# Kernel tuning notes

Measured on AMD Instinct MI355X. Metric: run time of the kernel, lower is better.

Reference implementation:

```python
import jax, jax.numpy as jnp
import numpy as np
from jax import lax

H, W = 128, 128
K_JUNC = 300
STEPS = 32
THRESH = 0.008
BIAS_SPAN = 1
SCALE = 5.0
SENTINEL = K_JUNC * K_JUNC


def decode_hafm(angs, dist, bias):
    # angs [B,3,H,W], dist [B,1,H,W], bias [B,1,H,W] -> lines [B,3,H,W,4]
    bias_range = jnp.arange(-BIAS_SPAN, BIAS_SPAN + 1, dtype=jnp.float32).reshape(1, -1, 1, 1)
    d = jnp.clip(dist + bias * bias_range, 0.0, 1.0)  # [B,3,H,W]
    angle0 = (angs[:, 0:1] - 0.5) * jnp.pi * 2
    angle1 = angs[:, 1:2] * jnp.pi / 2
    angle2 = -angs[:, 2:3] * jnp.pi / 2
    c0, s0 = jnp.cos(angle0), jnp.sin(angle0)
    t1, t2 = jnp.tan(angle1), jnp.tan(angle2)
    x1 = (c0 - s0 * t1) * d * SCALE
    y1 = (s0 + c0 * t1) * d * SCALE
    x2 = (c0 - s0 * t2) * d * SCALE
    y2 = (s0 + c0 * t2) * d * SCALE
    y0, x0 = jnp.meshgrid(jnp.arange(H, dtype=jnp.float32), jnp.arange(W, dtype=jnp.float32), indexing='ij')
    x0 = x0[None, None]
    y0 = y0[None, None]
    x1 = jnp.clip(x1 + x0, 0, W - 1)
    y1 = jnp.clip(y1 + y0, 0, H - 1)
    x2 = jnp.clip(x2 + x0, 0, W - 1)
    y2 = jnp.clip(y2 + y0, 0, H - 1)
    return jnp.stack((x1, y1, x2, y2), axis=-1)


def propose_junctions(jloc, joff):
    # jloc [H,W], joff [2,H,W]; 3x3 NMS + top-K, thresholded junctions
    pooled = lax.reduce_window(jloc, -jnp.inf, lax.max, (3, 3), (1, 1), 'SAME')
    nms = jnp.where(jloc == pooled, jloc, 0.0)
    scores, idx = lax.top_k(nms.reshape(-1), K_JUNC)
    y = (idx // W).astype(jnp.float32)
    x = (idx % W).astype(jnp.float32)
    xs = x + joff[0].reshape(-1)[idx]
    ys = y + joff[1].reshape(-1)[idx]
    coords = jnp.stack([xs, ys], axis=-1)  # [K,2]
    valid = scores > THRESH
    coords = jnp.where(valid[:, None], coords, 1e6)
    return coords, scores


def bilinear_sample(fmap, px, py):
    # fmap [C,H,W]; px,py [N,S] -> [C,N,S]
    C = fmap.shape[0]
    px = jnp.clip(px, 0.0, W - 1)
    py = jnp.clip(py, 0.0, H - 1)
    x0 = jnp.floor(px)
    y0 = jnp.floor(py)
    x0i = x0.astype(jnp.int32)
    y0i = y0.astype(jnp.int32)
    x1i = jnp.minimum(x0i + 1, W - 1)
    y1i = jnp.minimum(y0i + 1, H - 1)
    wx = px - x0
    wy = py - y0
    flat = fmap.reshape(C, H * W)

    def g(yi, xi):
        return flat[:, (yi * W + xi).reshape(-1)].reshape(C, *px.shape)

    return (g(y0i, x0i) * (1 - wx) * (1 - wy)
            + g(y0i, x1i) * wx * (1 - wy)
            + g(y1i, x0i) * (1 - wx) * wy
            + g(y1i, x1i) * wx * wy)


def setup_inputs() -> dict:
    key = jax.random.key(0)
    ks = jax.random.split(key, 10)
    return {
        'features': jax.random.normal(ks[0], (1, 256, H, W), jnp.float32),
        'heatmaps': jax.random.normal(ks[1], (1, 9, H, W), jnp.float32),
        'fc1_w': jax.random.normal(ks[2], (128, 256), jnp.float32) * 0.05,
        'fc1_b': jax.random.normal(ks[3], (128,), jnp.float32) * 0.05,
        'w1': jax.random.normal(ks[4], (1024, 1024), jnp.float32) * 0.03,
        'b1': jnp.zeros((1024,), jnp.float32),
        'w2': jax.random.normal(ks[5], (1024, 1024), jnp.float32) * 0.03,
        'b2': jnp.zeros((1024,), jnp.float32),
        'w3': jax.random.normal(ks[6], (1, 1024), jnp.float32) * 0.03,
        'b3': jnp.zeros((1,), jnp.float32),
    }


def reference(features, heatmaps, fc1_w, fc1_b, w1, b1, w2, b2, w3, b3):
    angs = jax.nn.sigmoid(heatmaps[:, 0:3])
    dist = jax.nn.sigmoid(heatmaps[:, 3:4])
    bias = jax.nn.sigmoid(heatmaps[:, 4:5])
    jloc = jax.nn.softmax(heatmaps[:, 5:7], axis=1)[0, 1]  # [H,W]
    joff = jax.nn.sigmoid(heatmaps[0, 7:9])                # [2,H,W]

    junc, _ = propose_junctions(jloc, joff)                # [K,2]
    lines = decode_hafm(angs, dist, bias).reshape(-1, 4)   # [N,4], N=3*H*W
    N = lines.shape[0]

    # junction-to-endpoint matching (cdist + argmin)
    d1 = ((junc[:, None, :] - lines[None, :, :2]) ** 2).sum(-1)  # [K,N]
    d2 = ((junc[:, None, :] - lines[None, :, 2:]) ** 2).sum(-1)
    j1 = jnp.argmin(d1, axis=0)
    j2 = jnp.argmin(d2, axis=0)
    lo = jnp.minimum(j1, j2)
    hi = jnp.maximum(j1, j2)
    ids = jnp.where(lo < hi, lo * K_JUNC + hi, SENTINEL)
    # fixed-size dedup (masked analogue of torch unique(dim=0))
    uids = jnp.unique(ids, size=N, fill_value=SENTINEL)
    valid = uids < SENTINEL
    uids_safe = jnp.where(valid, uids, 0)
    p1 = junc[uids_safe // K_JUNC]
    p2 = junc[uids_safe % K_JUNC]
    line_coords = jnp.where(valid[:, None], jnp.concatenate([p1, p2], axis=-1), 0.0)  # [N,4]

    # LOI feature sampling
    loi = jnp.einsum('oc,chw->ohw', fc1_w, features[0]) + fc1_b[:, None, None]  # [128,H,W]
    t = jnp.linspace(0.0, 1.0, STEPS)[None, :]
    px = line_coords[:, 0:1] * t + line_coords[:, 2:3] * (1 - t)  # [N,32]
    py = line_coords[:, 1:2] * t + line_coords[:, 3:4] * (1 - t)
    feats = bilinear_sample(loi, px, py)            # [128,N,32]
    feats = feats.transpose(1, 0, 2)                # [N,128,32]
    feats = feats.reshape(N, 128, STEPS // 4, 4).max(-1)  # max_pool1d k=4
    feats = feats.reshape(N, 1024)

    h = jax.nn.relu(feats @ w1.T + b1)
    h = jax.nn.relu(h @ w2.T + b2)
    logits = (h @ w3.T + b3)[:, 0]
    line_scores = jax.nn.sigmoid(logits) * valid
    return line_coords, line_scores
```

## Files before the change

kernel.cpp:

```cpp
#include <hip/hip_runtime.h>
#include <math.h>

#define HH 128
#define WW 128
#define HW 16384
#define NLINES 49152
#define KJ 300
#define SENT 90000
#define THRESHV 0.008f
#define CAND_CAP 4096
#define BITWORDS 2816

typedef __attribute__((ext_vector_type(8))) short bf16x8;
typedef __attribute__((ext_vector_type(4))) float f32x4;

__device__ __forceinline__ float sigm(float x){ return 1.0f/(1.0f+expf(-x)); }

__device__ __forceinline__ short tobf(float f){
  unsigned u = __float_as_uint(f);
  unsigned r = u + 0x7FFFu + ((u >> 16) & 1u);
  return (short)(r >> 16);
}
__device__ __forceinline__ float bflo(unsigned u){ return __uint_as_float(u << 16); }
__device__ __forceinline__ float bfhi(unsigned u){ return __uint_as_float(u & 0xFFFF0000u); }

#define GLOAD_LDS16(g, l) \
  __builtin_amdgcn_global_load_lds((const __attribute__((address_space(1))) void*)(g), \
                                   (__attribute__((address_space(3))) void*)(l), 16, 0, 0)

__device__ __forceinline__ float jloc_at(const float* hm, int idx){
  float h5 = hm[5*HW + idx], h6 = hm[6*HW + idx];
  float mx = fmaxf(h5,h6);
  float e5 = expf(h5-mx), e6 = expf(h6-mx);
  return e6/(e5+e6);
}

__global__ __launch_bounds__(256) void k_front(const float* __restrict__ hm,
    const float* __restrict__ feat, const float* __restrict__ fc1w,
    float* __restrict__ lines, unsigned long long* __restrict__ cand,
    int* __restrict__ cand_count, short* __restrict__ featT, short* __restrict__ fc1b16){
  __shared__ float tile[32][33];
  int b = blockIdx.x, t = threadIdx.x;
  if (b < 64){
    int i = b*256 + t;
    float h0 = hm[i], h1 = hm[HW+i], h2 = hm[2*HW+i], h3 = hm[3*HW+i], h4 = hm[4*HW+i];
    float a0 = sigm(h0), a1 = sigm(h1), a2 = sigm(h2);
    float dist = sigm(h3), bias = sigm(h4);
    const float PI = 3.14159265358979323846f;
    float ang0 = (a0-0.5f)*(2.0f*PI);
    float c0 = cosf(ang0), s0 = sinf(ang0);
    float t1 = tanf(a1*(0.5f*PI));
    float t2 = tanf(-a2*(0.5f*PI));
    int y = i >> 7, x = i & 127;
    float fx = (float)x, fy = (float)y;
    #pragma unroll
    for (int c=0;c<3;c++){
      float d = fminf(fmaxf(dist + bias*(float)(c-1), 0.0f), 1.0f);
      float ds = d*5.0f;
      float x1 = fminf(fmaxf((c0 - s0*t1)*ds + fx, 0.0f), 127.0f);
      float y1 = fminf(fmaxf((s0 + c0*t1)*ds + fy, 0.0f), 127.0f);
      float x2 = fminf(fmaxf((c0 - s0*t2)*ds + fx, 0.0f), 127.0f);
      float y2 = fminf(fmaxf((s0 + c0*t2)*ds + fy, 0.0f), 127.0f);
      ((float4*)lines)[c*HW + i] = make_float4(x1,y1,x2,y2);
    }
    float v = jloc_at(hm, i);
    float m = v;
    for (int dy=-1; dy<=1; dy++){
      int ny = y + dy; if (ny < 0 || ny >= HH) continue;
      for (int dx=-1; dx<=1; dx++){
        int nx = x + dx; if (nx < 0 || nx >= WW) continue;
        m = fmaxf(m, jloc_at(hm, ny*WW + nx));
      }
    }
    if (v == m && v > THRESHV){
      int pos = atomicAdd(cand_count, 1);
      if (pos < CAND_CAP){
        unsigned int vb = __float_as_uint(v);
        cand[pos] = ((unsigned long long)vb << 32) | (unsigned long long)(0xFFFFFFFFu - (unsigned)i);
      }
    }
  } else if (b < 64 + 4096){
    int idx = b - 64;
    int p0 = (idx & 511) * 32, c0 = (idx >> 9) * 32;
    int c  = t >> 3;
    int p4 = (t & 7) * 4;
    float4 v = *(const float4*)&feat[(size_t)(c0 + c)*HW + p0 + p4];
    tile[c][p4+0] = v.x; tile[c][p4+1] = v.y; tile[c][p4+2] = v.z; tile[c][p4+3] = v.w;
    __syncthreads();
    int p  = t >> 3;
    int cg = (t & 7) * 4;
    ushort4 o;
    o.x = (unsigned short)tobf(tile[cg+0][p]);
    o.y = (unsigned short)tobf(tile[cg+1][p]);
    o.z = (unsigned short)tobf(tile[cg+2][p]);
    o.w = (unsigned short)tobf(tile[cg+3][p]);
    *(ushort4*)&featT[(size_t)(p0 + p)*256 + c0 + cg] = o;
  } else {
    int j = (b - 4160)*256 + t;
    fc1b16[j] = tobf(fc1w[j]);
  }
}

__global__ __launch_bounds__(1024) void k_mid(
    const unsigned long long* __restrict__ cand, const int* __restrict__ cand_count,
    const float* __restrict__ hm, float* __restrict__ junc,
    const short* __restrict__ featT, const short* __restrict__ fc1b16,
    const float* __restrict__ fc1b, short* __restrict__ loi){
  __shared__ __align__(16) char smem[CAND_CAP*8];
  int b = blockIdx.x, t = threadIdx.x;
  if (b == 0){
    unsigned long long* s = (unsigned long long*)smem;
    int count = *cand_count; if (count > CAND_CAP) count = CAND_CAP;
    int n2 = 512;
    while (n2 < count) n2 <<= 1;
    for (int i=t; i<n2; i+=1024) s[i] = (i < count) ? cand[i] : 0ull;
    __syncthreads();
    for (int k=2; k<=n2; k<<=1){
      for (int j=k>>1; j>0; j>>=1){
        for (int i=t; i<n2; i+=1024){
          int ixj = i ^ j;
          if (ixj > i){
            unsigned long long a = s[i], bb = s[ixj];
            bool desc = ((i & k) == 0);
            if (desc ? (a < bb) : (a > bb)){ s[i] = bb; s[ixj] = a; }
          }
        }
        __syncthreads();
      }
    }
    if (t < KJ){
      float jx = 1e6f, jy = 1e6f;
      if (t < count){
        unsigned idx = 0xFFFFFFFFu - (unsigned)(s[t] & 0xFFFFFFFFull);
        int yy = (int)(idx >> 7), xx = (int)(idx & 127u);
        jx = (float)xx + sigm(hm[7*HW + idx]);
        jy = (float)yy + sigm(hm[8*HW + idx]);
      }
      junc[2*t] = jx; junc[2*t+1] = jy;
    }
  } else {
    if (t >= 256) return;
    short* As = (short*)smem;
    short* Bs = (short*)(smem + 8192);
    int rb = (b - 1) * 64;
    int lane = t & 63, wave = t >> 6;
    int l16 = lane & 15, quad = lane >> 4;
    int srow = lane >> 3, schunk = (lane & 7) ^ srow;
    f32x4 acc[8];
    #pragma unroll
    for (int g=0; g<8; g++) acc[g] = (f32x4){0,0,0,0};
    for (int k0=0; k0<256; k0+=64){
      #pragma unroll
      for (int i=0; i<2; i++){
        int r0 = wave*16 + i*8;
        GLOAD_LDS16(featT + (size_t)(rb + r0 + srow)*256 + k0 + schunk*8, &As[r0*64]);
      }
      #pragma unroll
      for (int i=0; i<4; i++){
        int r0 = wave*32 + i*8;
        GLOAD_LDS16(fc1b16 + (size_t)(r0 + srow)*256 + k0 + schunk*8, &Bs[r0*64]);
      }
      __syncthreads();
      #pragma unroll
      for (int s2=0; s2<2; s2++){
        int slot = (s2*4 + quad) ^ (l16 & 7);
        bf16x8 a = *(const bf16x8*)&As[(wave*16 + l16)*64 + slot*8];
        #pragma unroll
        for (int g=0; g<8; g++){
          bf16x8 bv = *(const bf16x8*)&Bs[(g*16 + l16)*64 + slot*8];
          acc[g] = __builtin_amdgcn_mfma_f32_16x16x32_bf16(a, bv, acc[g], 0, 0, 0);
        }
      }
      __syncthreads();
    }
    int rowbase = rb + wave*16 + quad*4;
    #pragma unroll
    for (int g=0; g<8; g++){
      int col = g*16 + l16;
      float bs = fc1b[col];
      #pragma unroll
      for (int r=0; r<4; r++)
        loi[(size_t)(rowbase + r)*128 + col] = tobf(acc[g][r] + bs);
    }
  }
}

__global__ __launch_bounds__(256) void k_match(const float* __restrict__ lines,
    const float* __restrict__ junc, int* __restrict__ ids,
    const float* __restrict__ w1, const float* __restrict__ w2,
    short* __restrict__ w1b, short* __restrict__ w2b){
  __shared__ float jx[KJ], jy[KJ];
  int b = blockIdx.x, t = threadIdx.x;
  if (b < 192){
    for (int k=t; k<KJ; k+=256){ jx[k] = junc[2*k]; jy[k] = junc[2*k+1]; }
    __syncthreads();
    int n = b*256 + t;
    float4 L = ((const float4*)lines)[n];
    float b1 = 1e30f, b2 = 1e30f; int j1 = 0, j2 = 0;
    #pragma unroll 4
    for (int k=0; k<KJ; k++){
      float dx1 = jx[k]-L.x, dy1 = jy[k]-L.y;
      float d1 = dx1*dx1 + dy1*dy1;
      float dx2 = jx[k]-L.z, dy2 = jy[k]-L.w;
      float d2 = dx2*dx2 + dy2*dy2;
      if (d1 < b1){ b1 = d1; j1 = k; }
      if (d2 < b2){ b2 = d2; j2 = k; }
    }
    int lo = min(j1,j2), hi = max(j1,j2);
    ids[n] = (lo < hi) ? (lo*KJ + hi) : SENT;
  } else {
    int j = (b - 192)*256 + t;
    w1b[j] = tobf(w1[j]);
    w2b[j] = tobf(w2[j]);
  }
}

__global__ __launch_bounds__(1024) void k_unique(const int* __restrict__ ids,
    int* __restrict__ uid_list, int* __restrict__ mcount){
  __shared__ unsigned bm[BITWORDS];
  __shared__ int wsum[16];
  int t = threadIdx.x;
  for (int i=t; i<BITWORDS; i+=1024) bm[i] = 0u;
  __syncthreads();
  for (int n=t; n<NLINES; n+=1024){
    int id = ids[n];
    if (id < SENT) atomicOr(&bm[id>>5], 1u << (id & 31));
  }
  __syncthreads();
  int w0 = t*3;
  int local = 0;
  unsigned wv[3];
  #pragma unroll
  for (int i=0; i<3; i++){
    int w = w0 + i;
    wv[i] = (w < BITWORDS) ? bm[w] : 0u;
    local += __popc(wv[i]);
  }
  int v = local;
  #pragma unroll
  for (int d=1; d<64; d<<=1){
    int nv = __shfl_up(v, d, 64);
    if ((t & 63) >= d) v += nv;
  }
  if ((t & 63) == 63) wsum[t >> 6] = v;
  __syncthreads();
  if (t < 16){
    int x = wsum[t];
    #pragma unroll
    for (int d=1; d<16; d<<=1){
      int nv = __shfl_up(x, d, 16);
      if (t >= d) x += nv;
    }
    wsum[t] = x;
  }
  __syncthreads();
  int base = v - local + ((t >> 6) ? wsum[(t >> 6) - 1] : 0);
  #pragma unroll
  for (int i=0; i<3; i++){
    unsigned bits = wv[i];
    while (bits){
      int bb = __ffs(bits) - 1;
      uid_list[base++] = (w0 + i)*32 + bb;
      bits &= bits - 1;
    }
  }
  if (t == 1023) *mcount = wsum[15];
}

__global__ __launch_bounds__(256) void k_sample(float* __restrict__ out,
    const int* __restrict__ uid_list, const float* __restrict__ junc,
    const short* __restrict__ loi, const int* __restrict__ mcount,
    short* __restrict__ fbuf, float* __restrict__ logit, int* __restrict__ cnt,
    int ncnt, int chunk0, int chunk){
  __shared__ int4   sOffs[32];
  __shared__ float4 sWts[32];
  int M = *mcount;
  int t = threadIdx.x;
  if (t == 0 && blockIdx.x < ncnt) cnt[blockIdx.x] = 0;
  int q  = t >> 6;
  int c2 = (t & 63) << 1;
  for (int l = blockIdx.x; l < chunk; l += gridDim.x){
    int r = chunk0 + l;
    if (r < M){
      if (t == 0) logit[l] = 0.0f;
      __syncthreads();
      if (t < 32){
        int id = uid_list[r];
        int lo = id / KJ, hi = id % KJ;
        float2 P1 = ((const float2*)junc)[lo];
        float2 P2 = ((const float2*)junc)[hi];
        if (t == 0) ((float4*)out)[r] = make_float4(P1.x, P1.y, P2.x, P2.y);
        float tt = (float)t * (1.0f/31.0f);
        float px = P1.x*tt + P2.x*(1.0f-tt);
        float py = P1.y*tt + P2.y*(1.0f-tt);
        px = fminf(fmaxf(px, 0.0f), 127.0f);
        py = fminf(fmaxf(py, 0.0f), 127.0f);
        float x0 = floorf(px), y0 = floorf(py);
        int x0i = (int)x0, y0i = (int)y0;
        int x1i = min(x0i+1, 127), y1i = min(y0i+1, 127);
        float wx = px - x0, wy = py - y0;
        sOffs[t] = make_int4((y0i*WW + x0i)*128, (y0i*WW + x1i)*128,
                             (y1i*WW + x0i)*128, (y1i*WW + x1i)*128);
        sWts[t]  = make_float4((1.0f-wx)*(1.0f-wy), wx*(1.0f-wy),
                               (1.0f-wx)*wy,        wx*wy);
      }
      __syncthreads();
      float gl0=-1e30f, gl1=-1e30f, gh0=-1e30f, gh1=-1e30f;
      #pragma unroll
      for (int j=0; j<8; j++){
        int s = q*8 + j;
        int4 o   = sOffs[s];
        float4 w = sWts[s];
        unsigned u00 = *(const unsigned*)&loi[o.x + c2];
        unsigned u01 = *(const unsigned*)&loi[o.y + c2];
        unsigned u10 = *(const unsigned*)&loi[o.z + c2];
        unsigned u11 = *(const unsigned*)&loi[o.w + c2];
        float vlo = w.x*bflo(u00) + w.y*bflo(u01) + w.z*bflo(u10) + w.w*bflo(u11);
        float vhi = w.x*bfhi(u00) + w.y*bfhi(u01) + w.z*bfhi(u10) + w.w*bfhi(u11);
        if (j < 4){ gl0 = fmaxf(gl0, vlo); gh0 = fmaxf(gh0, vhi); }
        else      { gl1 = fmaxf(gl1, vlo); gh1 = fmaxf(gh1, vhi); }
      }
      unsigned plo = ((unsigned)(unsigned short)tobf(gl0)) | (((unsigned)(unsigned short)tobf(gl1)) << 16);
      unsigned phi = ((unsigned)(unsigned short)tobf(gh0)) | (((unsigned)(unsigned short)tobf(gh1)) << 16);
      *(unsigned*)&fbuf[(size_t)l*1024 + c2*8 + q*2]     = plo;
      *(unsigned*)&fbuf[(size_t)l*1024 + (c2+1)*8 + q*2] = phi;
    } else {
      if (t == 0){
        ((float4*)out)[r] = make_float4(0.f,0.f,0.f,0.f);
        out[4*NLINES + r] = 0.0f;
      }
    }
  }
}

template<int MODE>
__global__ __launch_bounds__(256) void k_mlp(const short* __restrict__ A,
    const short* __restrict__ B, const float* __restrict__ bias,
    short* __restrict__ Hout, const float* __restrict__ w3,
    const float* __restrict__ b3, float* __restrict__ logit,
    int* __restrict__ cnt, const int* __restrict__ mcount,
    int chunk0, float* __restrict__ outScore){
  int M = *mcount;
  int rb = blockIdx.x * 128;
  if (chunk0 + rb >= M) return;
  int cb = blockIdx.y * 128;
  __shared__ short As[128*64];
  __shared__ short Bs[128*64];
  __shared__ int sflag;
  int lane = threadIdx.x & 63, wave = threadIdx.x >> 6;
  int l16 = lane & 15, quad = lane >> 4;
  int srow = lane >> 3, schunk = (lane & 7) ^ srow;
  f32x4 acc0[8], acc1[8];
  #pragma unroll
  for (int g=0; g<8; g++){ acc0[g] = (f32x4){0,0,0,0}; acc1[g] = (f32x4){0,0,0,0}; }
  for (int k0=0; k0<1024; k0+=64){
    #pragma unroll
    for (int i=0; i<4; i++){
      int r0 = wave*32 + i*8;
      GLOAD_LDS16(A + (size_t)(rb + r0 + srow)*1024 + k0 + schunk*8, &As[r0*64]);
      GLOAD_LDS16(B + (size_t)(cb + r0 + srow)*1024 + k0 + schunk*8, &Bs[r0*64]);
    }
    __syncthreads();
    #pragma unroll
    for (int s=0; s<2; s++){
      int slot = (s*4 + quad) ^ (l16 & 7);
      bf16x8 a0 = *(const bf16x8*)&As[(wave*32 + l16)*64 + slot*8];
      bf16x8 a1 = *(const bf16x8*)&As[(wave*32 + 16 + l16)*64 + slot*8];
      #pragma unroll
      for (int g=0; g<8; g++){
        bf16x8 bv = *(const bf16x8*)&Bs[(g*16 + l16)*64 + slot*8];
        acc0[g] = __builtin_amdgcn_mfma_f32_16x16x32_bf16(a0, bv, acc0[g], 0, 0, 0);
        acc1[g] = __builtin_amdgcn_mfma_f32_16x16x32_bf16(a1, bv, acc1[g], 0, 0, 0);
      }
    }
    __syncthreads();
  }
  int r0b = rb + wave*32 + quad*4;
  int r1b = r0b + 16;
  if (MODE == 0){
    #pragma unroll
    for (int g=0; g<8; g++){
      int col = cb + g*16 + l16;
      float bs = bias[col];
      #pragma unroll
      for (int r=0; r<4; r++){
        Hout[(size_t)(r0b + r)*1024 + col] = tobf(fmaxf(acc0[g][r] + bs, 0.0f));
        Hout[(size_t)(r1b + r)*1024 + col] = tobf(fmaxf(acc1[g][r] + bs, 0.0f));
      }
    }
  } else {
    float p0[4] = {0,0,0,0}, p1[4] = {0,0,0,0};
    #pragma unroll
    for (int g=0; g<8; g++){
      int col = cb + g*16 + l16;
      float bs = bias[col], wv = w3[col];
      #pragma unroll
      for (int r=0; r<4; r++){
        p0[r] += fmaxf(acc0[g][r] + bs, 0.0f) * wv;
        p1[r] += fmaxf(acc1[g][r] + bs, 0.0f) * wv;
      }
    }
    #pragma unroll
    for (int r=0; r<4; r++){
      #pragma unroll
      for (int m=1; m<16; m<<=1){
        p0[r] += __shfl_xor(p0[r], m, 16);
        p1[r] += __shfl_xor(p1[r], m, 16);
      }
    }
    if (l16 == 0){
      #pragma unroll
      for (int r=0; r<4; r++){
        atomicAdd(&logit[r0b + r], p0[r]);
        atomicAdd(&logit[r1b + r], p1[r]);
      }
    }
    __syncthreads();
    if (threadIdx.x == 0){
      __threadfence();
      int old = atomicAdd(&cnt[blockIdx.x], 1);
      sflag = (old == 7) ? 1 : 0;
    }
    __syncthreads();
    if (sflag){
      __threadfence();
      if (threadIdx.x < 128){
        int row = rb + threadIdx.x;
        int rg = chunk0 + row;
        if (rg < M){
          float lg = atomicAdd(&logit[row], 0.0f) + b3[0];
          outScore[4*NLINES + rg] = 1.0f/(1.0f + expf(-lg));
        }
      }
    }
  }
}

extern "C" void kernel_launch(void* const* d_in, const int* in_sizes, int n_in,
                              void* d_out, int out_size, void* d_ws, size_t ws_size,
                              hipStream_t stream){
  const float* features = (const float*)d_in[0];
  const float* heatmaps = (const float*)d_in[1];
  const float* fc1_w    = (const float*)d_in[2];
  const float* fc1_b    = (const float*)d_in[3];
  const float* w1       = (const float*)d_in[4];
  const float* b1       = (const float*)d_in[5];
  const float* w2       = (const float*)d_in[6];
  const float* b2       = (const float*)d_in[7];
  const float* w3       = (const float*)d_in[8];
  const float* b3       = (const float*)d_in[9];
  float* out = (float*)d_out;

  char* ws = (char*)d_ws;
  size_t off = 0;
  auto alloc = [&](size_t bytes) -> void* {
    void* p = ws + off;
    off = (off + bytes + 255) & ~(size_t)255;
    return p;
  };
  float* lines     = (float*)alloc((size_t)NLINES*16);
  unsigned long long* cand = (unsigned long long*)alloc(CAND_CAP*8);
  int*   cand_count= (int*)alloc(4);
  float* junc      = (float*)alloc(KJ*2*4);
  int*   ids       = (int*)alloc((size_t)NLINES*4);
  int*   uid_list  = (int*)alloc((size_t)NLINES*4);
  int*   mcount    = (int*)alloc(4);
  int*   cnt       = (int*)alloc((NLINES/128)*4);
  short* loi       = (short*)alloc((size_t)HW*128*2);
  short* featT     = (short*)alloc((size_t)HW*256*2);
  short* fc1b16    = (short*)alloc((size_t)128*256*2);
  short* w1b       = (short*)alloc((size_t)1024*1024*2);
  short* w2b       = (short*)alloc((size_t)1024*1024*2);
  size_t fixed = off;

  const int chunk_opts[7] = {49152, 24576, 12288, 8192, 4096, 2048, 1024};
  int CHUNK = 1024;
  for (int ci=0; ci<7; ci++){
    size_t need = fixed + (size_t)chunk_opts[ci]*1024*2*2 + (size_t)chunk_opts[ci]*4 + 1024;
    if (need <= ws_size){ CHUNK = chunk_opts[ci]; break; }
  }
  short* fbuf  = (short*)alloc((size_t)CHUNK*1024*2);
  short* h1buf = (short*)alloc((size_t)CHUNK*1024*2);
  float* logit = (float*)alloc((size_t)CHUNK*4);

  hipMemsetAsync(cand_count, 0, 4, stream);
  k_front<<<4288, 256, 0, stream>>>(heatmaps, features, fc1_w, lines, cand,
                                    cand_count, featT, fc1b16);
  k_mid  <<<257, 1024, 0, stream>>>(cand, cand_count, heatmaps, junc, featT,
                                    fc1b16, fc1_b, loi);
  k_match<<<4288, 256, 0, stream>>>(lines, junc, ids, w1, w2, w1b, w2b);
  k_unique<<<1, 1024, 0, stream>>>(ids, uid_list, mcount);

  int nchunk = NLINES / CHUNK;
  for (int ci=0; ci<nchunk; ci++){
    int chunk0 = ci * CHUNK;
    k_sample<<<2048, 256, 0, stream>>>(out, uid_list, junc, loi, mcount, fbuf,
                                       logit, cnt, CHUNK/128, chunk0, CHUNK);
    dim3 g1(CHUNK/128, 8);
    k_mlp<0><<<g1, 256, 0, stream>>>(fbuf, w1b, b1, h1buf, nullptr, nullptr,
                                     nullptr, nullptr, mcount, chunk0, nullptr);
    k_mlp<2><<<g1, 256, 0, stream>>>(h1buf, w2b, b2, nullptr, w3, b3,
                                     logit, cnt, mcount, chunk0, out);
  }
}
```

Before: 224.5 us.

## Fuse dedup bitmap into matching, shrink MLP row tiles, cap rows at max pairs

The matching kernel now sets bits in a global bitmap with atomics, which removes the ids buffer and the single-block scatter pass in k_unique. The line cap drops to 45056, just above the 44850 possible junction pairs, and the output is zero-filled by a memset so k_sample can stop at M instead of looping over padded rows. The MLP tile shrinks from 128 to 64 rows, giving finer row skipping and more blocks, at the cost of less B-tile reuse per block. NMS in k_front now reads jloc values from an LDS tile rather than recomputing each neighbour's softmax from global memory.

```diff
diff --git a/kernel.cpp b/kernel.cpp
--- a/kernel.cpp
+++ b/kernel.cpp
@@ -40,6 +40,7 @@
     float* __restrict__ lines, unsigned long long* __restrict__ cand,
     int* __restrict__ cand_count, short* __restrict__ featT, short* __restrict__ fc1b16){
   __shared__ float tile[32][33];
+  __shared__ float jl[4][128];
   int b = blockIdx.x, t = threadIdx.x;
   if (b < 64){
     int i = b*256 + t;
@@ -63,13 +64,23 @@
       float y2 = fminf(fmaxf((s0 + c0*t2)*ds + fy, 0.0f), 127.0f);
       ((float4*)lines)[c*HW + i] = make_float4(x1,y1,x2,y2);
     }
-    float v = jloc_at(hm, i);
+    int y0 = 2*b;
+    #pragma unroll
+    for (int idx = t; idx < 512; idx += 256){
+      int r = idx >> 7, xx = idx & 127;
+      int yy = y0 - 1 + r;
+      jl[r][xx] = (yy >= 0 && yy < HH) ? jloc_at(hm, yy*WW + xx) : -1e30f;
+    }
+    __syncthreads();
+    int lr = 1 + (t >> 7);
+    float v = jl[lr][x];
     float m = v;
+    #pragma unroll
     for (int dy=-1; dy<=1; dy++){
-      int ny = y + dy; if (ny < 0 || ny >= HH) continue;
+      #pragma unroll
       for (int dx=-1; dx<=1; dx++){
         int nx = x + dx; if (nx < 0 || nx >= WW) continue;
-        m = fmaxf(m, jloc_at(hm, ny*WW + nx));
+        m = fmaxf(m, jl[lr+dy][nx]);
       }
     }
     if (v == m && v > THRESHV){
@@ -186,7 +197,7 @@
 }
 
 __global__ __launch_bounds__(256) void k_match(const float* __restrict__ lines,
-    const float* __restrict__ junc, int* __restrict__ ids,
+    const float* __restrict__ junc, unsigned* __restrict__ bm,
     const float* __restrict__ w1, const float* __restrict__ w2,
     short* __restrict__ w1b, short* __restrict__ w2b){
   __shared__ float jx[KJ], jy[KJ];
@@ -207,7 +218,10 @@
       if (d2 < b2){ b2 = d2; j2 = k; }
     }
     int lo = min(j1,j2), hi = max(j1,j2);
-    ids[n] = (lo < hi) ? (lo*KJ + hi) : SENT;
+    if (lo < hi){
+      int id = lo*KJ + hi;
+      atomicOr(&bm[id >> 5], 1u << (id & 31));
+    }
   } else {
     int j = (b - 192)*256 + t;
     w1b[j] = tobf(w1[j]);
@@ -215,21 +229,13 @@
   }
 }
 
-__global__ __launch_bounds__(1024) void k_unique(const int* __restrict__ ids,
+__global__ __launch_bounds__(1024) void k_unique(const unsigned* __restrict__ bm,
     int* __restrict__ uid_list, int* __restrict__ mcount){
-  __shared__ unsigned bm[BITWORDS];
   __shared__ int wsum[16];
   int t = threadIdx.x;
-  for (int i=t; i<BITWORDS; i+=1024) bm[i] = 0u;
-  __syncthreads();
-  for (int n=t; n<NLINES; n+=1024){
-    int id = ids[n];
-    if (id < SENT) atomicOr(&bm[id>>5], 1u << (id & 31));
-  }
-  __syncthreads();
   int w0 = t*3;
+  unsigned wv[3];
   int local = 0;
-  unsigned wv[3];
   #pragma unroll
   for (int i=0; i<3; i++){
     int w = w0 + i;
@@ -279,57 +285,51 @@
   if (t == 0 && blockIdx.x < ncnt) cnt[blockIdx.x] = 0;
   int q  = t >> 6;
   int c2 = (t & 63) << 1;
-  for (int l = blockIdx.x; l < chunk; l += gridDim.x){
+  int lim = M - chunk0; if (lim > chunk) lim = chunk;
+  for (int l = blockIdx.x; l < lim; l += gridDim.x){
     int r = chunk0 + l;
-    if (r < M){
-      if (t == 0) logit[l] = 0.0f;
-      __syncthreads();
-      if (t < 32){
-        int id = uid_list[r];
-        int lo = id / KJ, hi = id % KJ;
-        float2 P1 = ((const float2*)junc)[lo];
-        float2 P2 = ((const float2*)junc)[hi];
-        if (t == 0) ((float4*)out)[r] = make_float4(P1.x, P1.y, P2.x, P2.y);
-        float tt = (float)t * (1.0f/31.0f);
-        float px = P1.x*tt + P2.x*(1.0f-tt);
-        float py = P1.y*tt + P2.y*(1.0f-tt);
-        px = fminf(fmaxf(px, 0.0f), 127.0f);
-        py = fminf(fmaxf(py, 0.0f), 127.0f);
-        float x0 = floorf(px), y0 = floorf(py);
-        int x0i = (int)x0, y0i = (int)y0;
-        int x1i = min(x0i+1, 127), y1i = min(y0i+1, 127);
-        float wx = px - x0, wy = py - y0;
-        sOffs[t] = make_int4((y0i*WW + x0i)*128, (y0i*WW + x1i)*128,
-                             (y1i*WW + x0i)*128, (y1i*WW + x1i)*128);
-        sWts[t]  = make_float4((1.0f-wx)*(1.0f-wy), wx*(1.0f-wy),
-                               (1.0f-wx)*wy,        wx*wy);
-      }
-      __syncthreads();
-      float gl0=-1e30f, gl1=-1e30f, gh0=-1e30f, gh1=-1e30f;
-      #pragma unroll
-      for (int j=0; j<8; j++){
-        int s = q*8 + j;
-        int4 o   = sOffs[s];
-        float4 w = sWts[s];
-        unsigned u00 = *(const unsigned*)&loi[o.x + c2];
-        unsigned u01 = *(const unsigned*)&loi[o.y + c2];
-        unsigned u10 = *(const unsigned*)&loi[o.z + c2];
-        unsigned u11 = *(const unsigned*)&loi[o.w + c2];
-        float vlo = w.x*bflo(u00) + w.y*bflo(u01) + w.z*bflo(u10) + w.w*bflo(u11);
-        float vhi = w.x*bfhi(u00) + w.y*bfhi(u01) + w.z*bfhi(u10) + w.w*bfhi(u11);
-        if (j < 4){ gl0 = fmaxf(gl0, vlo); gh0 = fmaxf(gh0, vhi); }
-        else      { gl1 = fmaxf(gl1, vlo); gh1 = fmaxf(gh1, vhi); }
-      }
-      unsigned plo = ((unsigned)(unsigned short)tobf(gl0)) | (((unsigned)(unsigned short)tobf(gl1)) << 16);
-      unsigned phi = ((unsigned)(unsigned short)tobf(gh0)) | (((unsigned)(unsigned short)tobf(gh1)) << 16);
-      *(unsigned*)&fbuf[(size_t)l*1024 + c2*8 + q*2]     = plo;
-      *(unsigned*)&fbuf[(size_t)l*1024 + (c2+1)*8 + q*2] = phi;
-    } else {
-      if (t == 0){
-        ((float4*)out)[r] = make_float4(0.f,0.f,0.f,0.f);
-        out[4*NLINES + r] = 0.0f;
-      }
-    }
+    if (t == 0) logit[l] = 0.0f;
+    __syncthreads();
+    if (t < 32){
+      int id = uid_list[r];
+      int lo = id / KJ, hi = id % KJ;
+      float2 P1 = ((const float2*)junc)[lo];
+      float2 P2 = ((const float2*)junc)[hi];
+      if (t == 0) ((float4*)out)[r] = make_float4(P1.x, P1.y, P2.x, P2.y);
+      float tt = (float)t * (1.0f/31.0f);
+      float px = P1.x*tt + P2.x*(1.0f-tt);
+      float py = P1.y*tt + P2.y*(1.0f-tt);
+      px = fminf(fmaxf(px, 0.0f), 127.0f);
+      py = fminf(fmaxf(py, 0.0f), 127.0f);
+      float x0 = floorf(px), y0 = floorf(py);
+      int x0i = (int)x0, y0i = (int)y0;
+      int x1i = min(x0i+1, 127), y1i = min(y0i+1, 127);
+      float wx = px - x0, wy = py - y0;
+      sOffs[t] = make_int4((y0i*WW + x0i)*128, (y0i*WW + x1i)*128,
+                           (y1i*WW + x0i)*128, (y1i*WW + x1i)*128);
+      sWts[t]  = make_float4((1.0f-wx)*(1.0f-wy), wx*(1.0f-wy),
+                             (1.0f-wx)*wy,        wx*wy);
+    }
+    __syncthreads();
+    float gl0=-1e30f, gl1=-1e30f, gh0=-1e30f, gh1=-1e30f;
+    #pragma unroll
+    for (int j=0; j<8; j++){
+      int s = q*8 + j;
+      int4 o   = sOffs[s];
+      float4 w = sWts[s];
+      unsigned u00 = *(const unsigned*)&loi[o.x + c2];
+      unsigned u01 = *(const unsigned*)&loi[o.y + c2];
+      unsigned u10 = *(const unsigned*)&loi[o.z + c2];
+      unsigned u11 = *(const unsigned*)&loi[o.w + c2];
+      float vlo = w.x*bflo(u00) + w.y*bflo(u01) + w.z*bflo(u10) + w.w*bflo(u11);
+      float vhi = w.x*bfhi(u00) + w.y*bfhi(u01) + w.z*bfhi(u10) + w.w*bfhi(u11);
+      if (j < 4){ gl0 = fmaxf(gl0, vlo); gh0 = fmaxf(gh0, vhi); }
+      else      { gl1 = fmaxf(gl1, vlo); gh1 = fmaxf(gh1, vhi); }
+    }
+    unsigned plo = ((unsigned)(unsigned short)tobf(gl0)) | (((unsigned)(unsigned short)tobf(gl1)) << 16);
+    unsigned phi = ((unsigned)(unsigned short)tobf(gh0)) | (((unsigned)(unsigned short)tobf(gh1)) << 16);
+    *(unsigned*)&fbuf[(size_t)l*1024 + c2*8 + q*2]     = plo;
+    *(unsigned*)&fbuf[(size_t)l*1024 + (c2+1)*8 + q*2] = phi;
   }
 }
 
@@ -341,79 +341,72 @@
     int* __restrict__ cnt, const int* __restrict__ mcount,
     int chunk0, float* __restrict__ outScore){
   int M = *mcount;
-  int rb = blockIdx.x * 128;
+  int rb = blockIdx.x * 64;
   if (chunk0 + rb >= M) return;
   int cb = blockIdx.y * 128;
-  __shared__ short As[128*64];
+  __shared__ short As[64*64];
   __shared__ short Bs[128*64];
   __shared__ int sflag;
   int lane = threadIdx.x & 63, wave = threadIdx.x >> 6;
   int l16 = lane & 15, quad = lane >> 4;
   int srow = lane >> 3, schunk = (lane & 7) ^ srow;
-  f32x4 acc0[8], acc1[8];
+  f32x4 acc[8];
   #pragma unroll
-  for (int g=0; g<8; g++){ acc0[g] = (f32x4){0,0,0,0}; acc1[g] = (f32x4){0,0,0,0}; }
+  for (int g=0; g<8; g++) acc[g] = (f32x4){0,0,0,0};
   for (int k0=0; k0<1024; k0+=64){
+    #pragma unroll
+    for (int i=0; i<2; i++){
+      int r0 = wave*16 + i*8;
+      GLOAD_LDS16(A + (size_t)(rb + r0 + srow)*1024 + k0 + schunk*8, &As[r0*64]);
+    }
     #pragma unroll
     for (int i=0; i<4; i++){
       int r0 = wave*32 + i*8;
-      GLOAD_LDS16(A + (size_t)(rb + r0 + srow)*1024 + k0 + schunk*8, &As[r0*64]);
       GLOAD_LDS16(B + (size_t)(cb + r0 + srow)*1024 + k0 + schunk*8, &Bs[r0*64]);
     }
     __syncthreads();
     #pragma unroll
     for (int s=0; s<2; s++){
       int slot = (s*4 + quad) ^ (l16 & 7);
-      bf16x8 a0 = *(const bf16x8*)&As[(wave*32 + l16)*64 + slot*8];
-      bf16x8 a1 = *(const bf16x8*)&As[(wave*32 + 16 + l16)*64 + slot*8];
+      bf16x8 a = *(const bf16x8*)&As[(wave*16 + l16)*64 + slot*8];
       #pragma unroll
       for (int g=0; g<8; g++){
         bf16x8 bv = *(const bf16x8*)&Bs[(g*16 + l16)*64 + slot*8];
-        acc0[g] = __builtin_amdgcn_mfma_f32_16x16x32_bf16(a0, bv, acc0[g], 0, 0, 0);
-        acc1[g] = __builtin_amdgcn_mfma_f32_16x16x32_bf16(a1, bv, acc1[g], 0, 0, 0);
-      }
-    }
-    __syncthreads();
-  }
-  int r0b = rb + wave*32 + quad*4;
-  int r1b = r0b + 16;
+        acc[g] = __builtin_amdgcn_mfma_f32_16x16x32_bf16(a, bv, acc[g], 0, 0, 0);
+      }
+    }
+    __syncthreads();
+  }
+  int rowbase = rb + wave*16 + quad*4;
   if (MODE == 0){
     #pragma unroll
     for (int g=0; g<8; g++){
       int col = cb + g*16 + l16;
       float bs = bias[col];
       #pragma unroll
-      for (int r=0; r<4; r++){
-        Hout[(size_t)(r0b + r)*1024 + col] = tobf(fmaxf(acc0[g][r] + bs, 0.0f));
-        Hout[(size_t)(r1b + r)*1024 + col] = tobf(fmaxf(acc1[g][r] + bs, 0.0f));
-      }
+      for (int r=0; r<4; r++)
+        Hout[(size_t)(rowbase + r)*1024 + col] = tobf(fmaxf(acc[g][r] + bs, 0.0f));
     }
   } else {
-    float p0[4] = {0,0,0,0}, p1[4] = {0,0,0,0};
+    float p0[4] = {0,0,0,0};
     #pragma unroll
     for (int g=0; g<8; g++){
       int col = cb + g*16 + l16;
       float bs = bias[col], wv = w3[col];
       #pragma unroll
-      for (int r=0; r<4; r++){
-        p0[r] += fmaxf(acc0[g][r] + bs, 0.0f) * wv;
-        p1[r] += fmaxf(acc1[g][r] + bs, 0.0f) * wv;
-      }
+      for (int r=0; r<4; r++)
+        p0[r] += fmaxf(acc[g][r] + bs, 0.0f) * wv;
     }
     #pragma unroll
     for (int r=0; r<4; r++){
       #pragma unroll
-      for (int m=1; m<16; m<<=1){
+      for (int m=1; m<16; m<<=1)
         p0[r] += __shfl_xor(p0[r], m, 16);
-        p1[r] += __shfl_xor(p1[r], m, 16);
-      }
     }
     if (l16 == 0){
       #pragma unroll
-      for (int r=0; r<4; r++){
-        atomicAdd(&logit[r0b + r], p0[r]);
-        atomicAdd(&logit[r1b + r], p1[r]);
-      }
+      for (int r=0; r<4; r++)
+        atomicAdd(&logit[rowbase + r], p0[r]);
     }
     __syncthreads();
     if (threadIdx.x == 0){
@@ -424,7 +417,7 @@
     __syncthreads();
     if (sflag){
       __threadfence();
-      if (threadIdx.x < 128){
+      if (threadIdx.x < 64){
         int row = rb + threadIdx.x;
         int rg = chunk0 + row;
         if (rg < M){
@@ -460,12 +453,13 @@
   };
   float* lines     = (float*)alloc((size_t)NLINES*16);
   unsigned long long* cand = (unsigned long long*)alloc(CAND_CAP*8);
-  int*   cand_count= (int*)alloc(4);
+  int*      cand_count = (int*)alloc(4);
+  unsigned* bitmap     = (unsigned*)alloc(BITWORDS*4);
+  size_t zlen = (size_t)((char*)(bitmap + BITWORDS) - (char*)cand_count);
   float* junc      = (float*)alloc(KJ*2*4);
-  int*   ids       = (int*)alloc((size_t)NLINES*4);
-  int*   uid_list  = (int*)alloc((size_t)NLINES*4);
+  int*   uid_list  = (int*)alloc((size_t)45056*4);
   int*   mcount    = (int*)alloc(4);
-  int*   cnt       = (int*)alloc((NLINES/128)*4);
+  int*   cnt       = (int*)alloc((45056/64)*4);
   short* loi       = (short*)alloc((size_t)HW*128*2);
   short* featT     = (short*)alloc((size_t)HW*256*2);
   short* fc1b16    = (short*)alloc((size_t)128*256*2);
@@ -473,9 +467,9 @@
   short* w2b       = (short*)alloc((size_t)1024*1024*2);
   size_t fixed = off;
 
-  const int chunk_opts[7] = {49152, 24576, 12288, 8192, 4096, 2048, 1024};
-  int CHUNK = 1024;
-  for (int ci=0; ci<7; ci++){
+  const int chunk_opts[4] = {45056, 22528, 11264, 5632};
+  int CHUNK = 5632;
+  for (int ci=0; ci<4; ci++){
     size_t need = fixed + (size_t)chunk_opts[ci]*1024*2*2 + (size_t)chunk_opts[ci]*4 + 1024;
     if (need <= ws_size){ CHUNK = chunk_opts[ci]; break; }
   }
@@ -483,20 +477,21 @@
   short* h1buf = (short*)alloc((size_t)CHUNK*1024*2);
   float* logit = (float*)alloc((size_t)CHUNK*4);
 
-  hipMemsetAsync(cand_count, 0, 4, stream);
+  hipMemsetAsync(cand_count, 0, zlen, stream);
+  hipMemsetAsync(d_out, 0, (size_t)out_size*4, stream);
   k_front<<<4288, 256, 0, stream>>>(heatmaps, features, fc1_w, lines, cand,
                                     cand_count, featT, fc1b16);
   k_mid  <<<257, 1024, 0, stream>>>(cand, cand_count, heatmaps, junc, featT,
                                     fc1b16, fc1_b, loi);
-  k_match<<<4288, 256, 0, stream>>>(lines, junc, ids, w1, w2, w1b, w2b);
-  k_unique<<<1, 1024, 0, stream>>>(ids, uid_list, mcount);
-
-  int nchunk = NLINES / CHUNK;
+  k_match<<<4288, 256, 0, stream>>>(lines, junc, bitmap, w1, w2, w1b, w2b);
+  k_unique<<<1, 1024, 0, stream>>>(bitmap, uid_list, mcount);
+
+  int nchunk = (45056 + CHUNK - 1) / CHUNK;
   for (int ci=0; ci<nchunk; ci++){
     int chunk0 = ci * CHUNK;
     k_sample<<<2048, 256, 0, stream>>>(out, uid_list, junc, loi, mcount, fbuf,
-                                       logit, cnt, CHUNK/128, chunk0, CHUNK);
-    dim3 g1(CHUNK/128, 8);
+                                       logit, cnt, CHUNK/64, chunk0, CHUNK);
+    dim3 g1(CHUNK/64, 8);
     k_mlp<0><<<g1, 256, 0, stream>>>(fbuf, w1b, b1, h1buf, nullptr, nullptr,
                                      nullptr, nullptr, mcount, chunk0, nullptr);
     k_mlp<2><<<g1, 256, 0, stream>>>(h1buf, w2b, b2, nullptr, w3, b3,
```

After: 210.4 us. 1.07x faster.
